# Performance work log

Hardware: AMD Instinct MI355X
Metric: run time of the kernel (lower is better)

The kernel has to match this reference:

```python
import jax, jax.numpy as jnp
import numpy as np

IN_FEATURES = 4096
LOCAL_FEATURES = 128
KERNEL_SIZE = 64
STRIDE = 32
FOLD_NUM = (IN_FEATURES - KERNEL_SIZE) // STRIDE + 1  # 127
BATCH = 4096


def setup_inputs() -> dict:
    key = jax.random.key(0)
    kx, kw, kb = jax.random.split(key, 3)
    x = jax.random.normal(kx, (BATCH, IN_FEATURES), dtype=jnp.float32)
    # Per-window linear weights: torch Linear weight is [out, in] = [local_features, kernel_size]
    bound = 1.0 / np.sqrt(KERNEL_SIZE)
    W = jax.random.uniform(kw, (FOLD_NUM, LOCAL_FEATURES, KERNEL_SIZE),
                           dtype=jnp.float32, minval=-bound, maxval=bound)
    b = jax.random.uniform(kb, (FOLD_NUM, LOCAL_FEATURES),
                           dtype=jnp.float32, minval=-bound, maxval=bound)
    return {"x": x, "W": W, "b": b}


def reference(x, W, b) -> jnp.ndarray:
    # Unfold: windows[f, k] = x[:, f*stride + k] -> [B, FOLD_NUM, KERNEL_SIZE]
    idx = jnp.arange(FOLD_NUM)[:, None] * STRIDE + jnp.arange(KERNEL_SIZE)[None, :]
    windows = x[:, idx]  # [B, F, K]
    # Batched per-window linear: out[b, f, l] = sum_k windows[b,f,k] * W[f,l,k] + b[f,l]
    out = jnp.einsum('bfk,flk->bfl', windows, W) + b[None, :, :]
    # torch.cat along dim 1 over fold index == reshape [B, F*L]
    return out.reshape(x.shape[0], FOLD_NUM * LOCAL_FEATURES)
```

## Files before the change

### kernel.cpp

```cpp
#include <hip/hip_runtime.h>
#include <hip/hip_bf16.h>

#define IN_F 4096
#define LOCAL_F 128
#define KSZ 64
#define STRIDE_ 32
#define FOLDS 127
#define BATCH_ 4096
#define OUT_F (FOLDS * LOCAL_F)
#define WN (FOLDS * LOCAL_F * KSZ)

typedef __attribute__((ext_vector_type(8))) short bf16x8;
typedef __attribute__((ext_vector_type(8))) unsigned short u16x8;
typedef __attribute__((ext_vector_type(4))) float f32x4;

__device__ __forceinline__ unsigned short f2bf(float f) {
    unsigned u = __builtin_bit_cast(unsigned, f);
    u += 0x7fffu + ((u >> 16) & 1u);
    return (unsigned short)(u >> 16);
}

__global__ __launch_bounds__(256)
void wprep_kernel(const float* __restrict__ W, unsigned short* __restrict__ Wbf) {
    int i = (blockIdx.x * 256 + threadIdx.x) * 8;
    if (i >= WN) return;
    float4 a = *reinterpret_cast<const float4*>(W + i);
    float4 c = *reinterpret_cast<const float4*>(W + i + 4);
    u16x8 s;
    s[0] = f2bf(a.x); s[1] = f2bf(a.y); s[2] = f2bf(a.z); s[3] = f2bf(a.w);
    s[4] = f2bf(c.x); s[5] = f2bf(c.y); s[6] = f2bf(c.z); s[7] = f2bf(c.w);
    *reinterpret_cast<u16x8*>(Wbf + i) = s;
}

__global__ __launch_bounds__(256, 4)
void ll_main(const float* __restrict__ x,
             const unsigned short* __restrict__ Wbf,
             const float* __restrict__ b,
             float* __restrict__ out) {
    const int rg = blockIdx.x;
    const int fq = blockIdx.y;
    const int row0 = rg * 16;

    const int wave = threadIdx.x >> 6;
    const int lane = threadIdx.x & 63;
    const int l16 = lane & 15;
    const int g   = lane >> 4;

    const float* xrow = x + (size_t)(row0 + l16) * IN_F + g * 8;
    float*       orow = out + (size_t)(row0 + l16) * OUT_F + 4 * g;

    const int ffirst = fq * 32 + wave;
    f32x4 nxa0, nxa1, nxb0, nxb1;
    {
        const float* p = xrow + ffirst * STRIDE_;
        nxa0 = *reinterpret_cast<const f32x4*>(p);
        nxa1 = *reinterpret_cast<const f32x4*>(p + 4);
        nxb0 = *reinterpret_cast<const f32x4*>(p + 32);
        nxb1 = *reinterpret_cast<const f32x4*>(p + 36);
    }

    #pragma unroll
    for (int j = 0; j < 8; ++j) {
        const int f = fq * 32 + wave + 4 * j;
        if (f >= FOLDS) break;

        f32x4 xa0 = nxa0, xa1 = nxa1, xb0 = nxb0, xb1 = nxb1;

        if (j < 7 && f + 4 < FOLDS) {
            const float* p = xrow + (f + 4) * STRIDE_;
            nxa0 = *reinterpret_cast<const f32x4*>(p);
            nxa1 = *reinterpret_cast<const f32x4*>(p + 4);
            nxb0 = *reinterpret_cast<const f32x4*>(p + 32);
            nxb1 = *reinterpret_cast<const f32x4*>(p + 36);
        }

        bf16x8 af0, af1;
        af0[0] = (short)f2bf(xa0[0]); af0[1] = (short)f2bf(xa0[1]);
        af0[2] = (short)f2bf(xa0[2]); af0[3] = (short)f2bf(xa0[3]);
        af0[4] = (short)f2bf(xa1[0]); af0[5] = (short)f2bf(xa1[1]);
        af0[6] = (short)f2bf(xa1[2]); af0[7] = (short)f2bf(xa1[3]);
        af1[0] = (short)f2bf(xb0[0]); af1[1] = (short)f2bf(xb0[1]);
        af1[2] = (short)f2bf(xb0[2]); af1[3] = (short)f2bf(xb0[3]);
        af1[4] = (short)f2bf(xb1[0]); af1[5] = (short)f2bf(xb1[1]);
        af1[6] = (short)f2bf(xb1[2]); af1[7] = (short)f2bf(xb1[3]);

        f32x4 acc[8];
        #pragma unroll
        for (int nt = 0; nt < 8; ++nt) acc[nt] = (f32x4){0.f, 0.f, 0.f, 0.f};

        const unsigned short* Wf = Wbf + (size_t)f * (LOCAL_F * KSZ) + l16 * KSZ + g * 8;
        {
            bf16x8 wf[8];
            #pragma unroll
            for (int nt = 0; nt < 8; ++nt)
                wf[nt] = *reinterpret_cast<const bf16x8*>(Wf + nt * 16 * KSZ);
            #pragma unroll
            for (int nt = 0; nt < 8; ++nt)
                acc[nt] = __builtin_amdgcn_mfma_f32_16x16x32_bf16(wf[nt], af0, acc[nt], 0, 0, 0);
        }
        {
            bf16x8 wf[8];
            #pragma unroll
            for (int nt = 0; nt < 8; ++nt)
                wf[nt] = *reinterpret_cast<const bf16x8*>(Wf + nt * 16 * KSZ + 32);
            #pragma unroll
            for (int nt = 0; nt < 8; ++nt)
                acc[nt] = __builtin_amdgcn_mfma_f32_16x16x32_bf16(wf[nt], af1, acc[nt], 0, 0, 0);
        }

        #pragma unroll
        for (int nt = 0; nt < 8; ++nt) {
            f32x4 bv = *reinterpret_cast<const f32x4*>(b + (size_t)f * LOCAL_F + nt * 16 + 4 * g);
            f32x4 v = acc[nt] + bv;
            __builtin_nontemporal_store(v,
                reinterpret_cast<f32x4*>(orow + (size_t)f * LOCAL_F + nt * 16));
        }
    }
}

extern "C" void kernel_launch(void* const* d_in, const int* in_sizes, int n_in,
                              void* d_out, int out_size, void* d_ws, size_t ws_size,
                              hipStream_t stream) {
    const float* x = (const float*)d_in[0];
    const float* W = (const float*)d_in[1];
    const float* b = (const float*)d_in[2];
    float* out = (float*)d_out;
    unsigned short* Wbf = (unsigned short*)d_ws;

    wprep_kernel<<<(WN / 8 + 255) / 256, 256, 0, stream>>>(W, Wbf);
    dim3 grid(BATCH_ / 16, 4);
    ll_main<<<grid, 256, 0, stream>>>(x, Wbf, b, out);
}
```

Before: 116.8 us.

## Stage bf16-converted x rows in LDS shared across all folds per block

```diff
diff --git a/kernel.cpp b/kernel.cpp
--- a/kernel.cpp
+++ b/kernel.cpp
@@ -9,6 +9,10 @@
 #define BATCH_ 4096
 #define OUT_F (FOLDS * LOCAL_F)
 #define WN (FOLDS * LOCAL_F * KSZ)
+
+#define ROWS 16
+#define LPAD 8
+#define LSTR (IN_F + LPAD)
 
 typedef __attribute__((ext_vector_type(8))) short bf16x8;
 typedef __attribute__((ext_vector_type(8))) unsigned short u16x8;
@@ -32,88 +36,77 @@
     *reinterpret_cast<u16x8*>(Wbf + i) = s;
 }
 
-__global__ __launch_bounds__(256, 4)
+__global__ __launch_bounds__(1024, 1)
 void ll_main(const float* __restrict__ x,
              const unsigned short* __restrict__ Wbf,
              const float* __restrict__ b,
              float* __restrict__ out) {
+    __shared__ unsigned short xs[ROWS][LSTR];
+
     const int rg = blockIdx.x;
-    const int fq = blockIdx.y;
-    const int row0 = rg * 16;
+    const int row0 = rg * ROWS;
+    const int t = threadIdx.x;
 
-    const int wave = threadIdx.x >> 6;
-    const int lane = threadIdx.x & 63;
-    const int l16 = lane & 15;
-    const int g   = lane >> 4;
+    #pragma unroll
+    for (int it = 0; it < 8; ++it) {
+        const int idx = it * 8192 + t * 8;
+        const int r = idx >> 12;
+        const int c = idx & 4095;
+        const float* p = x + (size_t)(row0 + r) * IN_F + c;
+        f32x4 a = *reinterpret_cast<const f32x4*>(p);
+        f32x4 d = *reinterpret_cast<const f32x4*>(p + 4);
+        u16x8 s;
+        s[0] = f2bf(a[0]); s[1] = f2bf(a[1]); s[2] = f2bf(a[2]); s[3] = f2bf(a[3]);
+        s[4] = f2bf(d[0]); s[5] = f2bf(d[1]); s[6] = f2bf(d[2]); s[7] = f2bf(d[3]);
+        *reinterpret_cast<u16x8*>(&xs[r][c]) = s;
+    }
+    __syncthreads();
 
-    const float* xrow = x + (size_t)(row0 + l16) * IN_F + g * 8;
+    const int w    = t >> 6;
+    const int lane = t & 63;
+    const int l16  = lane & 15;
+    const int g    = lane >> 4;
+
     float*       orow = out + (size_t)(row0 + l16) * OUT_F + 4 * g;
-
-    const int ffirst = fq * 32 + wave;
-    f32x4 nxa0, nxa1, nxb0, nxb1;
-    {
-        const float* p = xrow + ffirst * STRIDE_;
-        nxa0 = *reinterpret_cast<const f32x4*>(p);
-        nxa1 = *reinterpret_cast<const f32x4*>(p + 4);
-        nxb0 = *reinterpret_cast<const f32x4*>(p + 32);
-        nxb1 = *reinterpret_cast<const f32x4*>(p + 36);
-    }
 
     #pragma unroll
     for (int j = 0; j < 8; ++j) {
-        const int f = fq * 32 + wave + 4 * j;
-        if (f >= FOLDS) break;
+        const int f = w + 16 * j;
+        if (f < FOLDS) {
+            bf16x8 af0 = *reinterpret_cast<const bf16x8*>(&xs[l16][f * STRIDE_ + g * 8]);
+            bf16x8 af1 = *reinterpret_cast<const bf16x8*>(&xs[l16][f * STRIDE_ + 32 + g * 8]);
 
-        f32x4 xa0 = nxa0, xa1 = nxa1, xb0 = nxb0, xb1 = nxb1;
+            f32x4 acc[8];
+            #pragma unroll
+            for (int nt = 0; nt < 8; ++nt) acc[nt] = (f32x4){0.f, 0.f, 0.f, 0.f};
 
-        if (j < 7 && f + 4 < FOLDS) {
-            const float* p = xrow + (f + 4) * STRIDE_;
-            nxa0 = *reinterpret_cast<const f32x4*>(p);
-            nxa1 = *reinterpret_cast<const f32x4*>(p + 4);
-            nxb0 = *reinterpret_cast<const f32x4*>(p + 32);
-            nxb1 = *reinterpret_cast<const f32x4*>(p + 36);
-        }
+            const unsigned short* Wf = Wbf + (size_t)f * (LOCAL_F * KSZ) + l16 * KSZ + g * 8;
+            {
+                bf16x8 wf[8];
+                #pragma unroll
+                for (int nt = 0; nt < 8; ++nt)
+                    wf[nt] = *reinterpret_cast<const bf16x8*>(Wf + nt * 16 * KSZ);
+                #pragma unroll
+                for (int nt = 0; nt < 8; ++nt)
+                    acc[nt] = __builtin_amdgcn_mfma_f32_16x16x32_bf16(wf[nt], af0, acc[nt], 0, 0, 0);
+            }
+            {
+                bf16x8 wf[8];
+                #pragma unroll
+                for (int nt = 0; nt < 8; ++nt)
+                    wf[nt] = *reinterpret_cast<const bf16x8*>(Wf + nt * 16 * KSZ + 32);
+                #pragma unroll
+                for (int nt = 0; nt < 8; ++nt)
+                    acc[nt] = __builtin_amdgcn_mfma_f32_16x16x32_bf16(wf[nt], af1, acc[nt], 0, 0, 0);
+            }
 
-        bf16x8 af0, af1;
-        af0[0] = (short)f2bf(xa0[0]); af0[1] = (short)f2bf(xa0[1]);
-        af0[2] = (short)f2bf(xa0[2]); af0[3] = (short)f2bf(xa0[3]);
-        af0[4] = (short)f2bf(xa1[0]); af0[5] = (short)f2bf(xa1[1]);
-        af0[6] = (short)f2bf(xa1[2]); af0[7] = (short)f2bf(xa1[3]);
-        af1[0] = (short)f2bf(xb0[0]); af1[1] = (short)f2bf(xb0[1]);
-        af1[2] = (short)f2bf(xb0[2]); af1[3] = (short)f2bf(xb0[3]);
-        af1[4] = (short)f2bf(xb1[0]); af1[5] = (short)f2bf(xb1[1]);
-        af1[6] = (short)f2bf(xb1[2]); af1[7] = (short)f2bf(xb1[3]);
-
-        f32x4 acc[8];
-        #pragma unroll
-        for (int nt = 0; nt < 8; ++nt) acc[nt] = (f32x4){0.f, 0.f, 0.f, 0.f};
-
-        const unsigned short* Wf = Wbf + (size_t)f * (LOCAL_F * KSZ) + l16 * KSZ + g * 8;
-        {
-            bf16x8 wf[8];
             #pragma unroll
-            for (int nt = 0; nt < 8; ++nt)
-                wf[nt] = *reinterpret_cast<const bf16x8*>(Wf + nt * 16 * KSZ);
-            #pragma unroll
-            for (int nt = 0; nt < 8; ++nt)
-                acc[nt] = __builtin_amdgcn_mfma_f32_16x16x32_bf16(wf[nt], af0, acc[nt], 0, 0, 0);
-        }
-        {
-            bf16x8 wf[8];
-            #pragma unroll
-            for (int nt = 0; nt < 8; ++nt)
-                wf[nt] = *reinterpret_cast<const bf16x8*>(Wf + nt * 16 * KSZ + 32);
-            #pragma unroll
-            for (int nt = 0; nt < 8; ++nt)
-                acc[nt] = __builtin_amdgcn_mfma_f32_16x16x32_bf16(wf[nt], af1, acc[nt], 0, 0, 0);
-        }
-
-        #pragma unroll
-        for (int nt = 0; nt < 8; ++nt) {
-            f32x4 bv = *reinterpret_cast<const f32x4*>(b + (size_t)f * LOCAL_F + nt * 16 + 4 * g);
-            f32x4 v = acc[nt] + bv;
-            __builtin_nontemporal_store(v,
-                reinterpret_cast<f32x4*>(orow + (size_t)f * LOCAL_F + nt * 16));
+            for (int nt = 0; nt < 8; ++nt) {
+                f32x4 bv = *reinterpret_cast<const f32x4*>(b + (size_t)f * LOCAL_F + nt * 16 + 4 * g);
+                f32x4 v = acc[nt] + bv;
+                __builtin_nontemporal_store(v,
+                    reinterpret_cast<f32x4*>(orow + (size_t)f * LOCAL_F + nt * 16));
+            }
         }
     }
 }
@@ -128,6 +121,5 @@
     unsigned short* Wbf = (unsigned short*)d_ws;
 
     wprep_kernel<<<(WN / 8 + 255) / 256, 256, 0, stream>>>(W, Wbf);
-    dim3 grid(BATCH_ / 16, 4);
-    ll_main<<<grid, 256, 0, stream>>>(x, Wbf, b, out);
+    ll_main<<<dim3(256), 1024, 0, stream>>>(x, Wbf, b, out);
 }
```

Result: slower. 125.4 us (+7.4%).
